# Performance work log

Measured on AMD Instinct MI355X. Metric: run time of the kernel, lower is better.

Reference implementation:

```python
import jax, jax.numpy as jnp
import numpy as np


def setup_inputs() -> dict:
    key = jax.random.key(0)
    x = jax.random.normal(key, (32, 1024, 1024), dtype=jnp.float32)
    return {"x": x}


def reference(x) -> jnp.ndarray:
    # Orthonormal DCT-II along axis 1 via length-2n FFT of [x, reverse(x)],
    # matching tf dct_odd_case numerics (complex64 path, real part taken).
    N, n, m = x.shape
    nf = jnp.float32(n)
    # y = [x; flip(x, axis=1)] -> length 2n along axis 1
    y = jnp.concatenate([x, x[:, ::-1, :]], axis=1)
    F = jnp.fft.fft(y.astype(jnp.complex64), axis=1)[:, :n, :]  # [N, n, m] complex64
    k = jnp.arange(n, dtype=jnp.float32)
    # twiddle: exp(-i*pi*k/(2n)) / sqrt(2n), with k=0 term divided by sqrt(2)
    phase = -k * (jnp.pi / (2.0 * nf))
    t = (jnp.cos(phase) + 1j * jnp.sin(phase)).astype(jnp.complex64) / jnp.sqrt(2.0 * nf)
    scale0 = jnp.where(k == 0, 1.0 / jnp.sqrt(jnp.float32(2.0)), jnp.float32(1.0))
    t = t * scale0.astype(jnp.complex64)
    dct_x = jnp.real(t[None, :, None] * F)  # [N, n, m] float32
    return dct_x
```

## Files before the change

### kernel.cpp

```cpp
#include <hip/hip_runtime.h>
#include <hip/hip_bf16.h>
#include <math.h>

typedef __bf16 bf16_8 __attribute__((ext_vector_type(8)));
typedef float f32x4 __attribute__((ext_vector_type(4)));

#define NDIM 1024
#define BM 128
#define BN 128
#define BK 32
#define BSTRIDE 40

__device__ static inline void async_copy16(const void* g, void* l) {
  __builtin_amdgcn_global_load_lds(
      (__attribute__((address_space(1))) void*)g,
      (__attribute__((address_space(3))) void*)l, 16, 0, 0);
}

__global__ void gen_dct_mat(__bf16* __restrict__ C) {
  int idx = blockIdx.x * blockDim.x + threadIdx.x;
  int k = idx >> 10;
  int j = idx & 1023;
  int t = (k * (2 * j + 1)) & 4095;
  float ang = (float)t * 1.5339807878856412e-3f;
  float s = (k == 0) ? 0.03125f : 0.04419417382415922f;
  C[idx] = (__bf16)(s * cosf(ang));
}

__global__ __launch_bounds__(256) void dct_gemm(
    const float* __restrict__ x, const __bf16* __restrict__ A,
    float* __restrict__ out) {
  __shared__ __align__(64) __bf16 Asm[BM * BK];
  __shared__ __align__(64) __bf16 Bsm[BN * BSTRIDE];

  const int t = threadIdx.x;
  const int wave = t >> 6;
  const int lane = t & 63;
  const int bb = blockIdx.z;
  const int m0 = blockIdx.y * BM;
  const int n0 = blockIdx.x * BN;

  const __bf16* Ag0 =
      A + (size_t)(m0 + wave * 16 + (lane >> 2)) * NDIM + ((lane & 3) * 8);
  const __bf16* Ag1 = Ag0 + (size_t)64 * NDIM;
  __bf16* Al0 = Asm + (wave * 16) * BK;
  __bf16* Al1 = Asm + (64 + wave * 16) * BK;

  const int bc = t & 127;
  const int bjg = t >> 7;
  const float* xs =
      x + (size_t)bb * (NDIM * NDIM) + (size_t)(bjg * 16) * NDIM + (n0 + bc);
  bf16_8* bs0 = (bf16_8*)(Bsm + bc * BSTRIDE + bjg * 16);
  bf16_8* bs1 = (bf16_8*)(Bsm + bc * BSTRIDE + bjg * 16 + 8);

  const int row16 = lane & 15;
  const int kq8 = (lane >> 4) * 8;
  const int wm = (wave & 1) * 64;
  const int wn = (wave >> 1) * 64;

  f32x4 acc[4][4] = {};

  for (int k0 = 0; k0 < NDIM; k0 += BK) {
    __syncthreads();
    async_copy16(Ag0 + k0, Al0);
    async_copy16(Ag1 + k0, Al1);

    const float* xp = xs + (size_t)k0 * NDIM;
    bf16_8 v0, v1;
#pragma unroll
    for (int q = 0; q < 8; q++) {
      v0[q] = (__bf16)xp[(size_t)q * NDIM];
      v1[q] = (__bf16)xp[(size_t)(q + 8) * NDIM];
    }
    *bs0 = v0;
    *bs1 = v1;
    __syncthreads();

    bf16_8 af[4], bfr[4];
#pragma unroll
    for (int i = 0; i < 4; i++)
      af[i] = *(const bf16_8*)(Asm + (wm + i * 16 + row16) * BK + kq8);
#pragma unroll
    for (int j = 0; j < 4; j++)
      bfr[j] = *(const bf16_8*)(Bsm + (wn + j * 16 + row16) * BSTRIDE + kq8);
#pragma unroll
    for (int i = 0; i < 4; i++)
#pragma unroll
      for (int j = 0; j < 4; j++)
        acc[i][j] = __builtin_amdgcn_mfma_f32_16x16x32_bf16(af[i], bfr[j],
                                                            acc[i][j], 0, 0, 0);
  }

  float* ob = out + (size_t)bb * (NDIM * NDIM);
  const int rbase = (lane >> 4) * 4;
  const int cofs = lane & 15;
#pragma unroll
  for (int i = 0; i < 4; i++) {
#pragma unroll
    for (int r = 0; r < 4; r++) {
      int row = m0 + wm + i * 16 + rbase + r;
#pragma unroll
      for (int j = 0; j < 4; j++) {
        int col = n0 + wn + j * 16 + cofs;
        ob[(size_t)row * NDIM + col] = acc[i][j][r];
      }
    }
  }
}

extern "C" void kernel_launch(void* const* d_in, const int* in_sizes, int n_in,
                              void* d_out, int out_size, void* d_ws,
                              size_t ws_size, hipStream_t stream) {
  const float* x = (const float*)d_in[0];
  float* out = (float*)d_out;
  __bf16* Cmat = (__bf16*)d_ws;

  gen_dct_mat<<<dim3((NDIM * NDIM) / 256), dim3(256), 0, stream>>>(Cmat);

  dim3 grid(NDIM / BN, NDIM / BM, 32);
  dct_gemm<<<grid, dim3(256), 0, stream>>>(x, Cmat, out);
}
```

Measured before the change: 303.7 us.

## Pre-transpose and convert input to bf16 so GEMM loads both operands asynchronously

Adds a transpose+convert pass that writes x as bf16 in k-contiguous layout into workspace, so the GEMM can stream both A and B tiles with async global-to-LDS copies instead of strided scalar fp32 loads and in-register conversion. It chunks the batch by available workspace and falls back to the old fused kernel if the workspace is too small. The cost is an extra pass that reads x and writes a bf16 copy, plus extra kernel launches.

```diff
diff --git a/kernel.cpp b/kernel.cpp
--- a/kernel.cpp
+++ b/kernel.cpp
@@ -3,13 +3,12 @@
 #include <math.h>
 
 typedef __bf16 bf16_8 __attribute__((ext_vector_type(8)));
+typedef __bf16 bf16_4 __attribute__((ext_vector_type(4)));
 typedef float f32x4 __attribute__((ext_vector_type(4)));
 
 #define NDIM 1024
-#define BM 128
-#define BN 128
-#define BK 32
-#define BSTRIDE 40
+#define BATCH 32
+#define MAT_ELEMS (NDIM * NDIM)
 
 __device__ static inline void async_copy16(const void* g, void* l) {
   __builtin_amdgcn_global_load_lds(
@@ -27,31 +26,56 @@
   C[idx] = (__bf16)(s * cosf(ang));
 }
 
-__global__ __launch_bounds__(256) void dct_gemm(
-    const float* __restrict__ x, const __bf16* __restrict__ A,
+__global__ __launch_bounds__(256) void transpose_cvt(
+    const float* __restrict__ x, __bf16* __restrict__ xT) {
+  const int b = blockIdx.z;
+  const int tj = blockIdx.y * 64;
+  const int tc = blockIdx.x * 64;
+  const int t = threadIdx.x;
+  const int bj = t & 15;
+  const int bc = t >> 4;
+  const float* xp = x + (size_t)b * MAT_ELEMS +
+                    (size_t)(tj + bj * 4) * NDIM + (tc + bc * 4);
+  f32x4 v[4];
+#pragma unroll
+  for (int r = 0; r < 4; r++) v[r] = *(const f32x4*)(xp + (size_t)r * NDIM);
+  __bf16* op = xT + (size_t)b * MAT_ELEMS + (size_t)(tc + bc * 4) * NDIM +
+               (tj + bj * 4);
+#pragma unroll
+  for (int e = 0; e < 4; e++) {
+    bf16_4 w;
+    w[0] = (__bf16)v[0][e];
+    w[1] = (__bf16)v[1][e];
+    w[2] = (__bf16)v[2][e];
+    w[3] = (__bf16)v[3][e];
+    *(bf16_4*)(op + (size_t)e * NDIM) = w;
+  }
+}
+
+__global__ __launch_bounds__(256) void dct_gemm_bt(
+    const __bf16* __restrict__ A, const __bf16* __restrict__ B,
     float* __restrict__ out) {
-  __shared__ __align__(64) __bf16 Asm[BM * BK];
-  __shared__ __align__(64) __bf16 Bsm[BN * BSTRIDE];
+  __shared__ __align__(64) __bf16 Asm[128 * 32];
+  __shared__ __align__(64) __bf16 Bsm[128 * 32];
 
   const int t = threadIdx.x;
   const int wave = t >> 6;
   const int lane = t & 63;
   const int bb = blockIdx.z;
-  const int m0 = blockIdx.y * BM;
-  const int n0 = blockIdx.x * BN;
+  const int m0 = blockIdx.y * 128;
+  const int n0 = blockIdx.x * 128;
 
   const __bf16* Ag0 =
       A + (size_t)(m0 + wave * 16 + (lane >> 2)) * NDIM + ((lane & 3) * 8);
   const __bf16* Ag1 = Ag0 + (size_t)64 * NDIM;
-  __bf16* Al0 = Asm + (wave * 16) * BK;
-  __bf16* Al1 = Asm + (64 + wave * 16) * BK;
-
-  const int bc = t & 127;
-  const int bjg = t >> 7;
-  const float* xs =
-      x + (size_t)bb * (NDIM * NDIM) + (size_t)(bjg * 16) * NDIM + (n0 + bc);
-  bf16_8* bs0 = (bf16_8*)(Bsm + bc * BSTRIDE + bjg * 16);
-  bf16_8* bs1 = (bf16_8*)(Bsm + bc * BSTRIDE + bjg * 16 + 8);
+  const __bf16* Bg0 = B + (size_t)bb * MAT_ELEMS +
+                      (size_t)(n0 + wave * 16 + (lane >> 2)) * NDIM +
+                      ((lane & 3) * 8);
+  const __bf16* Bg1 = Bg0 + (size_t)64 * NDIM;
+  __bf16* Al0 = Asm + (wave * 16) * 32;
+  __bf16* Al1 = Asm + (64 + wave * 16) * 32;
+  __bf16* Bl0 = Bsm + (wave * 16) * 32;
+  __bf16* Bl1 = Bsm + (64 + wave * 16) * 32;
 
   const int row16 = lane & 15;
   const int kq8 = (lane >> 4) * 8;
@@ -60,7 +84,81 @@
 
   f32x4 acc[4][4] = {};
 
-  for (int k0 = 0; k0 < NDIM; k0 += BK) {
+  for (int k0 = 0; k0 < NDIM; k0 += 32) {
+    __syncthreads();
+    async_copy16(Ag0 + k0, Al0);
+    async_copy16(Ag1 + k0, Al1);
+    async_copy16(Bg0 + k0, Bl0);
+    async_copy16(Bg1 + k0, Bl1);
+    __syncthreads();
+
+    bf16_8 af[4], bfr[4];
+#pragma unroll
+    for (int i = 0; i < 4; i++)
+      af[i] = *(const bf16_8*)(Asm + (wm + i * 16 + row16) * 32 + kq8);
+#pragma unroll
+    for (int j = 0; j < 4; j++)
+      bfr[j] = *(const bf16_8*)(Bsm + (wn + j * 16 + row16) * 32 + kq8);
+#pragma unroll
+    for (int i = 0; i < 4; i++)
+#pragma unroll
+      for (int j = 0; j < 4; j++)
+        acc[i][j] = __builtin_amdgcn_mfma_f32_16x16x32_bf16(af[i], bfr[j],
+                                                            acc[i][j], 0, 0, 0);
+  }
+
+  float* ob = out + (size_t)bb * MAT_ELEMS;
+  const int rbase = (lane >> 4) * 4;
+  const int cofs = lane & 15;
+#pragma unroll
+  for (int i = 0; i < 4; i++) {
+#pragma unroll
+    for (int r = 0; r < 4; r++) {
+      int row = m0 + wm + i * 16 + rbase + r;
+#pragma unroll
+      for (int j = 0; j < 4; j++) {
+        int col = n0 + wn + j * 16 + cofs;
+        ob[(size_t)row * NDIM + col] = acc[i][j][r];
+      }
+    }
+  }
+}
+
+#define BSTRIDE 40
+__global__ __launch_bounds__(256) void dct_gemm_fused(
+    const float* __restrict__ x, const __bf16* __restrict__ A,
+    float* __restrict__ out) {
+  __shared__ __align__(64) __bf16 Asm[128 * 32];
+  __shared__ __align__(64) __bf16 Bsm[128 * BSTRIDE];
+
+  const int t = threadIdx.x;
+  const int wave = t >> 6;
+  const int lane = t & 63;
+  const int bb = blockIdx.z;
+  const int m0 = blockIdx.y * 128;
+  const int n0 = blockIdx.x * 128;
+
+  const __bf16* Ag0 =
+      A + (size_t)(m0 + wave * 16 + (lane >> 2)) * NDIM + ((lane & 3) * 8);
+  const __bf16* Ag1 = Ag0 + (size_t)64 * NDIM;
+  __bf16* Al0 = Asm + (wave * 16) * 32;
+  __bf16* Al1 = Asm + (64 + wave * 16) * 32;
+
+  const int bc = t & 127;
+  const int bjg = t >> 7;
+  const float* xs =
+      x + (size_t)bb * MAT_ELEMS + (size_t)(bjg * 16) * NDIM + (n0 + bc);
+  bf16_8* bs0 = (bf16_8*)(Bsm + bc * BSTRIDE + bjg * 16);
+  bf16_8* bs1 = (bf16_8*)(Bsm + bc * BSTRIDE + bjg * 16 + 8);
+
+  const int row16 = lane & 15;
+  const int kq8 = (lane >> 4) * 8;
+  const int wm = (wave & 1) * 64;
+  const int wn = (wave >> 1) * 64;
+
+  f32x4 acc[4][4] = {};
+
+  for (int k0 = 0; k0 < NDIM; k0 += 32) {
     __syncthreads();
     async_copy16(Ag0 + k0, Al0);
     async_copy16(Ag1 + k0, Al1);
@@ -79,7 +177,7 @@
     bf16_8 af[4], bfr[4];
 #pragma unroll
     for (int i = 0; i < 4; i++)
-      af[i] = *(const bf16_8*)(Asm + (wm + i * 16 + row16) * BK + kq8);
+      af[i] = *(const bf16_8*)(Asm + (wm + i * 16 + row16) * 32 + kq8);
 #pragma unroll
     for (int j = 0; j < 4; j++)
       bfr[j] = *(const bf16_8*)(Bsm + (wn + j * 16 + row16) * BSTRIDE + kq8);
@@ -91,7 +189,7 @@
                                                             acc[i][j], 0, 0, 0);
   }
 
-  float* ob = out + (size_t)bb * (NDIM * NDIM);
+  float* ob = out + (size_t)bb * MAT_ELEMS;
   const int rbase = (lane >> 4) * 4;
   const int cofs = lane & 15;
 #pragma unroll
@@ -114,9 +212,24 @@
   const float* x = (const float*)d_in[0];
   float* out = (float*)d_out;
   __bf16* Cmat = (__bf16*)d_ws;
-
-  gen_dct_mat<<<dim3((NDIM * NDIM) / 256), dim3(256), 0, stream>>>(Cmat);
-
-  dim3 grid(NDIM / BN, NDIM / BM, 32);
-  dct_gemm<<<grid, dim3(256), 0, stream>>>(x, Cmat, out);
-}
+  const size_t cbytes = (size_t)MAT_ELEMS * 2;
+
+  gen_dct_mat<<<dim3(MAT_ELEMS / 256), dim3(256), 0, stream>>>(Cmat);
+
+  size_t avail = ws_size > cbytes ? ws_size - cbytes : 0;
+  int nb = (int)(avail / cbytes);
+  if (nb > BATCH) nb = BATCH;
+
+  if (nb >= 1) {
+    __bf16* xT = (__bf16*)((char*)d_ws + cbytes);
+    for (int b0 = 0; b0 < BATCH; b0 += nb) {
+      int n = (BATCH - b0) < nb ? (BATCH - b0) : nb;
+      transpose_cvt<<<dim3(16, 16, n), dim3(256), 0, stream>>>(
+          x + (size_t)b0 * MAT_ELEMS, xT);
+      dct_gemm_bt<<<dim3(8, 8, n), dim3(256), 0, stream>>>(
+          Cmat, xT, out + (size_t)b0 * MAT_ELEMS);
+    }
+  } else {
+    dct_gemm_fused<<<dim3(8, 8, BATCH), dim3(256), 0, stream>>>(x, Cmat, out);
+  }
+}
```

Result: slower. 327.4 us (+7.8%).

## Double-buffer DCT matrix tiles, prefetch x into registers, swizzle A LDS layout

Applied to the files above, without the earlier changes.

Adds a second LDS buffer for the DCT-matrix tile so the async global-to-LDS copy of the next K-slice is issued before the current slice's MFMAs run. The fp32 input column values for the next slice are likewise loaded into registers during compute and converted to bf16 at the top of the next iteration, hiding global load latency. It also XOR-swizzles the A tile column placement to reduce LDS bank conflicts on fragment reads. This costs more LDS and 16 extra registers per thread, and the last iteration issues a wasted wrap-around prefetch.

```diff
diff --git a/kernel.cpp b/kernel.cpp
--- a/kernel.cpp
+++ b/kernel.cpp
@@ -6,9 +6,8 @@
 typedef float f32x4 __attribute__((ext_vector_type(4)));
 
 #define NDIM 1024
-#define BM 128
-#define BN 128
-#define BK 32
+#define BATCH 32
+#define MAT_ELEMS (NDIM * NDIM)
 #define BSTRIDE 40
 
 __device__ static inline void async_copy16(const void* g, void* l) {
@@ -27,59 +26,72 @@
   C[idx] = (__bf16)(s * cosf(ang));
 }
 
-__global__ __launch_bounds__(256) void dct_gemm(
+__global__ __launch_bounds__(256) void dct_fused(
     const float* __restrict__ x, const __bf16* __restrict__ A,
     float* __restrict__ out) {
-  __shared__ __align__(64) __bf16 Asm[BM * BK];
-  __shared__ __align__(64) __bf16 Bsm[BN * BSTRIDE];
+  __shared__ __align__(64) __bf16 Asm[2][128 * 32];
+  __shared__ __align__(64) __bf16 Bsm[128 * BSTRIDE];
 
   const int t = threadIdx.x;
   const int wave = t >> 6;
   const int lane = t & 63;
   const int bb = blockIdx.z;
-  const int m0 = blockIdx.y * BM;
-  const int n0 = blockIdx.x * BN;
+  const int m0 = blockIdx.y * 128;
+  const int n0 = blockIdx.x * 128;
 
+  const int asw = ((lane & 3) ^ ((lane >> 3) & 3)) * 8;
   const __bf16* Ag0 =
-      A + (size_t)(m0 + wave * 16 + (lane >> 2)) * NDIM + ((lane & 3) * 8);
+      A + (size_t)(m0 + wave * 16 + (lane >> 2)) * NDIM + asw;
   const __bf16* Ag1 = Ag0 + (size_t)64 * NDIM;
-  __bf16* Al0 = Asm + (wave * 16) * BK;
-  __bf16* Al1 = Asm + (64 + wave * 16) * BK;
+  const int al0 = (wave * 16) * 32;
+  const int al1 = (64 + wave * 16) * 32;
 
   const int bc = t & 127;
   const int bjg = t >> 7;
   const float* xs =
-      x + (size_t)bb * (NDIM * NDIM) + (size_t)(bjg * 16) * NDIM + (n0 + bc);
+      x + (size_t)bb * MAT_ELEMS + (size_t)(bjg * 16) * NDIM + (n0 + bc);
   bf16_8* bs0 = (bf16_8*)(Bsm + bc * BSTRIDE + bjg * 16);
   bf16_8* bs1 = (bf16_8*)(Bsm + bc * BSTRIDE + bjg * 16 + 8);
 
   const int row16 = lane & 15;
+  const int aksw = ((lane >> 4) ^ ((lane >> 1) & 3)) * 8;
   const int kq8 = (lane >> 4) * 8;
   const int wm = (wave & 1) * 64;
   const int wn = (wave >> 1) * 64;
 
   f32x4 acc[4][4] = {};
 
-  for (int k0 = 0; k0 < NDIM; k0 += BK) {
+  async_copy16(Ag0, (__bf16*)Asm[0] + al0);
+  async_copy16(Ag1, (__bf16*)Asm[0] + al1);
+  float f[16];
+#pragma unroll
+  for (int q = 0; q < 16; q++) f[q] = xs[(size_t)q * NDIM];
+
+  for (int k0 = 0; k0 < NDIM; k0 += 32) {
+    const int buf = (k0 >> 5) & 1;
     __syncthreads();
-    async_copy16(Ag0 + k0, Al0);
-    async_copy16(Ag1 + k0, Al1);
-
-    const float* xp = xs + (size_t)k0 * NDIM;
     bf16_8 v0, v1;
 #pragma unroll
     for (int q = 0; q < 8; q++) {
-      v0[q] = (__bf16)xp[(size_t)q * NDIM];
-      v1[q] = (__bf16)xp[(size_t)(q + 8) * NDIM];
+      v0[q] = (__bf16)f[q];
+      v1[q] = (__bf16)f[q + 8];
     }
     *bs0 = v0;
     *bs1 = v1;
     __syncthreads();
 
+    const int kn = (k0 + 32) & (NDIM - 1);
+    async_copy16(Ag0 + kn, (__bf16*)Asm[buf ^ 1] + al0);
+    async_copy16(Ag1 + kn, (__bf16*)Asm[buf ^ 1] + al1);
+    const float* xp = xs + (size_t)kn * NDIM;
+#pragma unroll
+    for (int q = 0; q < 16; q++) f[q] = xp[(size_t)q * NDIM];
+
+    const __bf16* Ab = (const __bf16*)Asm[buf];
     bf16_8 af[4], bfr[4];
 #pragma unroll
     for (int i = 0; i < 4; i++)
-      af[i] = *(const bf16_8*)(Asm + (wm + i * 16 + row16) * BK + kq8);
+      af[i] = *(const bf16_8*)(Ab + (wm + i * 16 + row16) * 32 + aksw);
 #pragma unroll
     for (int j = 0; j < 4; j++)
       bfr[j] = *(const bf16_8*)(Bsm + (wn + j * 16 + row16) * BSTRIDE + kq8);
@@ -91,7 +103,7 @@
                                                             acc[i][j], 0, 0, 0);
   }
 
-  float* ob = out + (size_t)bb * (NDIM * NDIM);
+  float* ob = out + (size_t)bb * MAT_ELEMS;
   const int rbase = (lane >> 4) * 4;
   const int cofs = lane & 15;
 #pragma unroll
@@ -115,8 +127,6 @@
   float* out = (float*)d_out;
   __bf16* Cmat = (__bf16*)d_ws;
 
-  gen_dct_mat<<<dim3((NDIM * NDIM) / 256), dim3(256), 0, stream>>>(Cmat);
-
-  dim3 grid(NDIM / BN, NDIM / BM, 32);
-  dct_gemm<<<grid, dim3(256), 0, stream>>>(x, Cmat, out);
+  gen_dct_mat<<<dim3(MAT_ELEMS / 256), dim3(256), 0, stream>>>(Cmat);
+  dct_fused<<<dim3(8, 8, BATCH), dim3(256), 0, stream>>>(x, Cmat, out);
 }
```

New measurement: 327.4 us. 1.08x slower.
